# Performance work log

Measured on AMD Instinct MI355X. Metric: run time of the kernel, lower is better.

The kernel has to match this reference:

```python
import jax, jax.numpy as jnp
import numpy as np

N, E, H, ED = 50000, 400000, 512, 64
BN_EPS = 1e-5


def setup_inputs() -> dict:
    key = jax.random.key(0)
    ks = jax.random.split(key, 8)
    s = lambda d: 1.0 / np.sqrt(d)
    return {
        "x": jax.random.normal(ks[0], (N, H), jnp.float32),
        "edge_attr": jax.random.normal(ks[1], (E, ED), jnp.float32),
        "edge_index": jax.random.randint(ks[2], (2, E), 0, N, jnp.int32),
        # GINEConv edge projection (edge_dim -> hidden_dim)
        "W_e": jax.random.normal(ks[3], (ED, H), jnp.float32) * s(ED),
        "b_e": jnp.zeros((H,), jnp.float32),
        # 2-layer MLP: Linear(H, 2H) -> BN -> SiLU -> Linear(2H, H)
        "W1": jax.random.normal(ks[4], (H, 2 * H), jnp.float32) * s(H),
        "b1": jnp.zeros((2 * H,), jnp.float32),
        "g1": jnp.ones((2 * H,), jnp.float32),
        "beta1": jnp.zeros((2 * H,), jnp.float32),
        "W2": jax.random.normal(ks[5], (2 * H, H), jnp.float32) * s(2 * H),
        "b2": jnp.zeros((H,), jnp.float32),
        # outer BatchNorm(hidden_dim)
        "g2": jnp.ones((H,), jnp.float32),
        "beta2": jnp.zeros((H,), jnp.float32),
        # trainable GIN epsilon (init 0)
        "eps": jnp.zeros((), jnp.float32),
    }


def _bn(h, g, b):
    # training-mode batch norm over the node dimension (biased variance)
    mu = jnp.mean(h, axis=0)
    var = jnp.mean(jnp.square(h - mu), axis=0)
    return (h - mu) * jax.lax.rsqrt(var + BN_EPS) * g + b


def reference(x, edge_attr, edge_index, W_e, b_e, W1, b1, g1, beta1, W2, b2, g2, beta2, eps):
    src, dst = edge_index[0], edge_index[1]
    # message: ReLU(x_j + lin(e_ij)), gathered per edge  -> [E, H]
    msg = jax.nn.relu(x[src] + edge_attr @ W_e + b_e)
    # scatter-add aggregate into destination nodes -> [N, H]
    aggr = jax.ops.segment_sum(msg, dst, num_segments=x.shape[0])
    # GIN combine + 2-layer MLP with internal BatchNorm + SiLU (dropout=0)
    h = (1.0 + eps) * x + aggr
    h = jax.nn.silu(_bn(h @ W1 + b1, g1, beta1))
    h = h @ W2 + b2
    # outer BatchNorm + SiLU (dropout=0 -> identity)
    return jax.nn.silu(_bn(h, g2, beta2))
```

## Files before the change

kernel.cpp:

```cpp
#include <hip/hip_runtime.h>
#include <math.h>

#define NN 50000
#define NE 400000
#define HD 512
#define EDIM 64
#define H2 1024
#define LDT 72
#define CAP_SLOT 1200000
#define CAP_TILE 75000
#define CAP_HEAVY 8192
#define NBLK_SCAN 98

typedef short s16x8 __attribute__((ext_vector_type(8)));
typedef float f32x4 __attribute__((ext_vector_type(4)));

__device__ __forceinline__ unsigned short f2bf(float f) {
    union { float f; unsigned u; } v; v.f = f;
    unsigned r = v.u + 0x7fffu + ((v.u >> 16) & 1u);
    return (unsigned short)(r >> 16);
}
__device__ __forceinline__ float bf2f(unsigned short h) {
    union { unsigned u; float f; } v; v.u = ((unsigned)h) << 16;
    return v.f;
}
__device__ __forceinline__ float silu_f(float t) {
    return t / (1.f + __expf(-t));
}

constexpr size_t OFF_AGGRC = 0;
constexpr size_t OFF_XB   = 16777216;
constexpr size_t OFF_H1   = 0;
constexpr size_t OFF_H    = 102400000;
constexpr size_t OFF_WET  = 153600000;
constexpr size_t OFF_W1T  = OFF_WET + 65536;
constexpr size_t OFF_W2T  = OFF_W1T + 1048576;
constexpr size_t OFF_CNT  = OFF_W2T + 1048576;
constexpr size_t OFF_B1S  = OFF_CNT + 200000;
constexpr size_t OFF_B1Q  = OFF_B1S + 4096;
constexpr size_t OFF_B2S  = OFF_B1Q + 4096;
constexpr size_t OFF_B2Q  = OFF_B2S + 2048;
constexpr size_t ZERO_BYTES = 200000 + 4096 + 4096 + 2048 + 2048;
constexpr size_t OFF_TEX  = OFF_B2Q + 2048;
constexpr size_t OFF_BSUM = OFF_TEX + 200000;
constexpr size_t OFF_BOFF = OFF_BSUM + 512;
constexpr size_t OFF_T    = OFF_BOFF + 512;
constexpr size_t OFF_CUR  = OFF_T + 64;
constexpr size_t OFF_NOT  = OFF_CUR + 200000;
constexpr size_t OFF_SRCP = OFF_NOT + 300032;
constexpr size_t OFF_EIXP = OFF_SRCP + 4800000;
constexpr size_t OFF_SC1  = OFF_EIXP + 4800000;
constexpr size_t OFF_SB1  = OFF_SC1 + 4096;
constexpr size_t OFF_SC2  = OFF_SB1 + 4096;
constexpr size_t OFF_SB2  = OFF_SC2 + 2048;

__global__ __launch_bounds__(256) void k_convert(const float* __restrict__ We,
    const float* __restrict__ W1, const float* __restrict__ W2,
    unsigned short* __restrict__ wet, unsigned short* __restrict__ w1t,
    unsigned short* __restrict__ w2t) {
    int i = blockIdx.x * 256 + threadIdx.x;
    if (i < 32768) {
        int n = i >> 6, k = i & 63;
        wet[i] = f2bf(We[k * HD + n]);
    } else if (i < 32768 + 524288) {
        int j = i - 32768;
        int n = j >> 9, k = j & 511;
        w1t[j] = f2bf(W1[k * H2 + n]);
    } else if (i < 32768 + 2 * 524288) {
        int j = i - (32768 + 524288);
        int n = j >> 10, k = j & 1023;
        w2t[j] = f2bf(W2[k * HD + n]);
    }
}

__global__ __launch_bounds__(256) void k_xconv(const float* __restrict__ x,
    unsigned short* __restrict__ xb) {
    int t = blockIdx.x * 256 + threadIdx.x;
    if (t >= NN * 64) return;
    int n = t >> 6, rem = t & 63;
    int cb = rem >> 4, l = rem & 15;
    const float* src = x + (size_t)n * HD + cb * 128 + l;
    unsigned short o[8];
    #pragma unroll
    for (int j = 0; j < 8; ++j) o[j] = f2bf(src[j * 16]);
    *(uint4*)(xb + (size_t)n * HD + cb * 128 + l * 8) = *(const uint4*)o;
}

__global__ __launch_bounds__(256) void k_hist(const int* __restrict__ dst, int* __restrict__ counts) {
    int e = blockIdx.x * 256 + threadIdx.x;
    if (e < NE) atomicAdd(&counts[dst[e]], 1);
}

__global__ __launch_bounds__(512) void k_scan1(const int* __restrict__ counts,
    int* __restrict__ tile_excl, int* __restrict__ bsum) {
    __shared__ int wsums[8];
    int b = blockIdx.x, t = threadIdx.x;
    int i = b * 512 + t;
    int v = (i < NN) ? ((counts[i] + 15) >> 4) : 0;
    int lane = t & 63, wid = t >> 6;
    int x = v;
    #pragma unroll
    for (int o = 1; o < 64; o <<= 1) {
        int y = __shfl_up(x, o, 64);
        if (lane >= o) x += y;
    }
    if (lane == 63) wsums[wid] = x;
    __syncthreads();
    if (t == 0) {
        int run = 0;
        for (int w = 0; w < 8; ++w) { int tmp = wsums[w]; wsums[w] = run; run += tmp; }
    }
    __syncthreads();
    int excl = x - v + wsums[wid];
    if (i < NN) tile_excl[i] = excl;
    if (t == 511) bsum[b] = excl + v;
}

__global__ void k_scan2(const int* __restrict__ bsum, int* __restrict__ boff, int* __restrict__ Tout) {
    if (threadIdx.x == 0) {
        int run = 0;
        for (int b = 0; b < NBLK_SCAN; ++b) { boff[b] = run; run += bsum[b]; }
        Tout[0] = run;
        Tout[1] = 0;
    }
}

__global__ __launch_bounds__(512) void k_scan3(const int* __restrict__ counts,
    int* __restrict__ tile_excl, const int* __restrict__ boff,
    int* __restrict__ cursor, int* __restrict__ node_of_tile, int* __restrict__ Tout) {
    int b = blockIdx.x, t = threadIdx.x;
    int i = b * 512 + t;
    if (i >= NN) return;
    int tc = (counts[i] + 15) >> 4;
    int ts = tile_excl[i] + boff[b];
    cursor[i] = ts * 16;
    int hid = -1;
    if (tc > 1) {
        hid = atomicAdd(&Tout[1], 1);
        if (hid >= CAP_HEAVY) hid = CAP_HEAVY - 1;
    }
    tile_excl[i] = hid;
    unsigned tag = (tc > 1) ? (0x80000000u | (unsigned)hid) : (unsigned)i;
    for (int k = 0; k < tc; ++k) node_of_tile[ts + k] = (int)tag;
}

__global__ __launch_bounds__(256) void k_scatter(const int* __restrict__ src, const int* __restrict__ dst,
    int* __restrict__ cursor, int* __restrict__ srcp, int* __restrict__ eidxp) {
    int e = blockIdx.x * 256 + threadIdx.x;
    if (e < NE) {
        int d = dst[e];
        int p = atomicAdd(&cursor[d], 1);
        srcp[p] = src[e];
        eidxp[p] = e;
    }
}

__global__ __launch_bounds__(256, 4) void k_edge(
    const float* __restrict__ ea, const unsigned short* __restrict__ wet,
    const unsigned short* __restrict__ xb, const float* __restrict__ b_e,
    const float* __restrict__ eps,
    const int* __restrict__ srcp, const int* __restrict__ eidxp,
    const int* __restrict__ node_of_tile, const int* __restrict__ Tptr,
    float* __restrict__ aggrc, unsigned short* __restrict__ h) {
    int tile0 = blockIdx.x * 2;
    int T = Tptr[0];
    if (tile0 >= T) return;
    __shared__ unsigned short As[32 * LDT];
    __shared__ int Ss[32];
    __shared__ float Rs[4][128];
    int t = threadIdx.x;
    int slot0 = tile0 * 16;
    {
        int r = t >> 3, qq = t & 7;
        int s = srcp[slot0 + r];
        if (qq == 0) Ss[r] = s;
        unsigned short* lp = As + r * LDT + qq * 8;
        if (s >= 0) {
            int eix = eidxp[slot0 + r];
            const float* gp = ea + (size_t)eix * EDIM + qq * 8;
            float4 v0 = ((const float4*)gp)[0];
            float4 v1 = ((const float4*)gp)[1];
            lp[0] = f2bf(v0.x); lp[1] = f2bf(v0.y); lp[2] = f2bf(v0.z); lp[3] = f2bf(v0.w);
            lp[4] = f2bf(v1.x); lp[5] = f2bf(v1.y); lp[6] = f2bf(v1.z); lp[7] = f2bf(v1.w);
        } else {
            uint4 z = {0u, 0u, 0u, 0u};
            *(uint4*)lp = z;
        }
    }
    __syncthreads();
    int wave = t >> 6, lane = t & 63, l15 = lane & 15, quad = lane >> 4;
    int cblk = wave * 128;
    f32x4 acc[2][8];
    #pragma unroll
    for (int i = 0; i < 2; ++i)
        #pragma unroll
        for (int j = 0; j < 8; ++j) acc[i][j] = (f32x4){0.f, 0.f, 0.f, 0.f};
    #pragma unroll
    for (int k0 = 0; k0 < 64; k0 += 32) {
        s16x8 af[2], bfr[8];
        #pragma unroll
        for (int i = 0; i < 2; ++i)
            af[i] = *(const s16x8*)(As + (i * 16 + l15) * LDT + k0 + quad * 8);
        #pragma unroll
        for (int j = 0; j < 8; ++j)
            bfr[j] = *(const s16x8*)(wet + (size_t)(cblk + j * 16 + l15) * EDIM + k0 + quad * 8);
        #pragma unroll
        for (int i = 0; i < 2; ++i)
            #pragma unroll
            for (int j = 0; j < 8; ++j)
                acc[i][j] = __builtin_amdgcn_mfma_f32_16x16x32_bf16(af[i], bfr[j], acc[i][j], 0, 0, 0);
    }
    float ep = 1.0f + eps[0];
    float bev[8];
    #pragma unroll
    for (int j = 0; j < 8; ++j) bev[j] = b_e[cblk + j * 16 + l15];
    float* rp = Rs[wave];
    #pragma unroll
    for (int i = 0; i < 2; ++i) {
        int tile = tile0 + i;
        unsigned meta = (unsigned)node_of_tile[tile];
        int v = (int)(meta & 0x7fffffffu);
        int vc = v < NN ? v : 0;
        int srow = i * 16 + quad * 4;
        s16x8 xr[4]; float msk[4];
        #pragma unroll
        for (int r = 0; r < 4; ++r) {
            int s = Ss[srow + r];
            msk[r] = s >= 0 ? 1.f : 0.f;
            xr[r] = *(const s16x8*)(xb + (size_t)(s >= 0 ? s : 0) * HD + cblk + l15 * 8);
        }
        s16x8 xo = *(const s16x8*)(xb + (size_t)vc * HD + cblk + l15 * 8);
        float sum8[8];
        #pragma unroll
        for (int j = 0; j < 8; ++j) sum8[j] = 0.f;
        #pragma unroll
        for (int r = 0; r < 4; ++r) {
            #pragma unroll
            for (int j = 0; j < 8; ++j) {
                float vv = acc[i][j][r] + bf2f((unsigned short)xr[r][j]) + bev[j];
                vv = vv > 0.f ? vv : 0.f;
                sum8[j] = fmaf(msk[r], vv, sum8[j]);
            }
        }
        #pragma unroll
        for (int j = 0; j < 8; ++j) {
            sum8[j] += __shfl_xor(sum8[j], 16, 64);
            sum8[j] += __shfl_xor(sum8[j], 32, 64);
        }
        if (tile < T) {
            if (meta & 0x80000000u) {
                if (quad == 0) {
                    float* ap = aggrc + (size_t)v * HD + cblk;
                    #pragma unroll
                    for (int j = 0; j < 8; ++j) atomicAdd(ap + j * 16 + l15, sum8[j]);
                }
            } else {
                int j0 = quad * 2, j1 = j0 + 1;
                rp[j0 * 16 + l15] = fmaf(ep, bf2f((unsigned short)xo[j0]), sum8[j0]);
                rp[j1 * 16 + l15] = fmaf(ep, bf2f((unsigned short)xo[j1]), sum8[j1]);
                unsigned pk = (unsigned)f2bf(rp[lane * 2]) |
                              ((unsigned)f2bf(rp[lane * 2 + 1]) << 16);
                *(unsigned*)(h + (size_t)v * HD + cblk + lane * 2) = pk;
            }
        }
    }
}

__global__ __launch_bounds__(256) void k_combine_heavy(const float* __restrict__ aggrc,
    const float* __restrict__ x, const int* __restrict__ counts, const int* __restrict__ hidmap,
    const float* __restrict__ eps, unsigned short* __restrict__ h) {
    long i = ((long)blockIdx.x * 256 + threadIdx.x) * 4;
    if (i >= (long)NN * HD) return;
    int v = (int)(i >> 9);
    int c = counts[v];
    if (c >= 1 && c <= 16) return;
    float ep = 1.0f + eps[0];
    float4 a = {0.f, 0.f, 0.f, 0.f};
    if (c > 16) a = *(const float4*)(aggrc + (size_t)hidmap[v] * HD + (i & (HD - 1)));
    float4 xv = *(const float4*)(x + i);
    uint2 p;
    p.x = (unsigned)f2bf(ep * xv.x + a.x) | ((unsigned)f2bf(ep * xv.y + a.y) << 16);
    p.y = (unsigned)f2bf(ep * xv.z + a.z) | ((unsigned)f2bf(ep * xv.w + a.w) << 16);
    *(uint2*)(h + i) = p;
}

template <bool BF16OUT, bool SILU_A>
__global__ __launch_bounds__(256) void k_gemm_bn(
    const unsigned short* __restrict__ A, const unsigned short* __restrict__ Bt,
    const float* __restrict__ bias, void* __restrict__ Cv,
    float* __restrict__ bn_sum, float* __restrict__ bn_sumsq,
    const float* __restrict__ a_sc, const float* __restrict__ a_sb,
    int M, int K, int Nn) {
    __shared__ unsigned short As[128 * LDT];
    __shared__ unsigned short Bs[128 * LDT];
    __shared__ float csum[128], csumsq[128];
    int mblk = blockIdx.x, nblk = blockIdx.y;
    int t = threadIdx.x;
    int row0 = mblk * 128, col0 = nblk * 128;
    int wid = t >> 6, lane = t & 63, l15 = lane & 15, quad = lane >> 4;
    f32x4 acc[2][8];
    #pragma unroll
    for (int i = 0; i < 2; ++i)
        #pragma unroll
        for (int j = 0; j < 8; ++j) acc[i][j] = (f32x4){0.f, 0.f, 0.f, 0.f};

    for (int k0 = 0; k0 < K; k0 += 64) {
        __syncthreads();
        {
            int r = t >> 1, half = t & 1;
            int row = row0 + r;
            int kb = k0 + half * 32;
            unsigned short* lp = As + r * LDT + half * 32;
            if (row < M) {
                const unsigned short* gp = A + (size_t)row * K + kb;
                if (SILU_A) {
                    #pragma unroll
                    for (int jj = 0; jj < 4; ++jj) {
                        uint4 u = *(const uint4*)(gp + jj * 8);
                        float4 sA = *(const float4*)(a_sc + kb + jj * 8);
                        float4 sB = *(const float4*)(a_sc + kb + jj * 8 + 4);
                        float4 bA = *(const float4*)(a_sb + kb + jj * 8);
                        float4 bB = *(const float4*)(a_sb + kb + jj * 8 + 4);
                        unsigned short o[8];
                        o[0] = f2bf(silu_f(bf2f((unsigned short)(u.x & 0xffffu)) * sA.x + bA.x));
                        o[1] = f2bf(silu_f(bf2f((unsigned short)(u.x >> 16)) * sA.y + bA.y));
                        o[2] = f2bf(silu_f(bf2f((unsigned short)(u.y & 0xffffu)) * sA.z + bA.z));
                        o[3] = f2bf(silu_f(bf2f((unsigned short)(u.y >> 16)) * sA.w + bA.w));
                        o[4] = f2bf(silu_f(bf2f((unsigned short)(u.z & 0xffffu)) * sB.x + bB.x));
                        o[5] = f2bf(silu_f(bf2f((unsigned short)(u.z >> 16)) * sB.y + bB.y));
                        o[6] = f2bf(silu_f(bf2f((unsigned short)(u.w & 0xffffu)) * sB.z + bB.z));
                        o[7] = f2bf(silu_f(bf2f((unsigned short)(u.w >> 16)) * sB.w + bB.w));
                        #pragma unroll
                        for (int m = 0; m < 8; ++m) lp[jj * 8 + m] = o[m];
                    }
                } else {
                    #pragma unroll
                    for (int jj = 0; jj < 4; ++jj) *(uint4*)(lp + jj * 8) = *(const uint4*)(gp + jj * 8);
                }
            } else {
                uint4 z = {0u, 0u, 0u, 0u};
                #pragma unroll
                for (int jj = 0; jj < 4; ++jj) *(uint4*)(lp + jj * 8) = z;
            }
            const unsigned short* gb = Bt + (size_t)(col0 + r) * K + kb;
            unsigned short* lb = Bs + r * LDT + half * 32;
            #pragma unroll
            for (int jj = 0; jj < 4; ++jj) *(uint4*)(lb + jj * 8) = *(const uint4*)(gb + jj * 8);
        }
        __syncthreads();
        #pragma unroll
        for (int kk = 0; kk < 64; kk += 32) {
            s16x8 af[2], bfr[8];
            #pragma unroll
            for (int i = 0; i < 2; ++i)
                af[i] = *(const s16x8*)(As + (wid * 32 + i * 16 + l15) * LDT + kk + quad * 8);
            #pragma unroll
            for (int j = 0; j < 8; ++j)
                bfr[j] = *(const s16x8*)(Bs + (j * 16 + l15) * LDT + kk + quad * 8);
            #pragma unroll
            for (int i = 0; i < 2; ++i)
                #pragma unroll
                for (int j = 0; j < 8; ++j)
                    acc[i][j] = __builtin_amdgcn_mfma_f32_16x16x32_bf16(af[i], bfr[j], acc[i][j], 0, 0, 0);
        }
    }
    if (t < 128) { csum[t] = 0.f; csumsq[t] = 0.f; }
    __syncthreads();
    int mrow0 = row0 + wid * 32;
    #pragma unroll
    for (int j = 0; j < 8; ++j) {
        int col = j * 16 + l15;
        float bv = bias[col0 + col];
        float ls = 0.f, lq = 0.f;
        #pragma unroll
        for (int i = 0; i < 2; ++i) {
            #pragma unroll
            for (int r = 0; r < 4; ++r) {
                int row = mrow0 + i * 16 + quad * 4 + r;
                if (row < M) {
                    float v = acc[i][j][r] + bv;
                    if (BF16OUT)
                        ((unsigned short*)Cv)[(size_t)row * Nn + col0 + col] = f2bf(v);
                    else
                        ((float*)Cv)[(size_t)row * Nn + col0 + col] = v;
                    ls += v; lq += v * v;
                }
            }
        }
        atomicAdd(&csum[col], ls);
        atomicAdd(&csumsq[col], lq);
    }
    __syncthreads();
    if (t < 128) {
        atomicAdd(bn_sum + col0 + t, csum[t]);
        atomicAdd(bn_sumsq + col0 + t, csumsq[t]);
    }
}

__global__ __launch_bounds__(256) void k_bn_final(const float* __restrict__ s,
    const float* __restrict__ q, const float* __restrict__ g, const float* __restrict__ beta,
    float* __restrict__ scale, float* __restrict__ sbias, int C, float invN) {
    int c = blockIdx.x * 256 + threadIdx.x;
    if (c < C) {
        float mu = s[c] * invN;
        float var = q[c] * invN - mu * mu;
        var = fmaxf(var, 0.f);
        float sc = g[c] * rsqrtf(var + 1e-5f);
        scale[c] = sc;
        sbias[c] = beta[c] - mu * sc;
    }
}

__global__ __launch_bounds__(256) void k_out(float* __restrict__ out,
    const float* __restrict__ sc, const float* __restrict__ sb, long total) {
    long i = ((long)blockIdx.x * 256 + threadIdx.x) * 4;
    if (i >= total) return;
    int c = (int)(i & (HD - 1));
    float4 v = *(const float4*)(out + i);
    float4 s4 = *(const float4*)(sc + c);
    float4 b4 = *(const float4*)(sb + c);
    float4 o;
    o.x = silu_f(v.x * s4.x + b4.x);
    o.y = silu_f(v.y * s4.y + b4.y);
    o.z = silu_f(v.z * s4.z + b4.z);
    o.w = silu_f(v.w * s4.w + b4.w);
    *(float4*)(out + i) = o;
}

extern "C" void kernel_launch(void* const* d_in, const int* in_sizes, int n_in,
                              void* d_out, int out_size, void* d_ws, size_t ws_size,
                              hipStream_t stream) {
    const float* x      = (const float*)d_in[0];
    const float* ea     = (const float*)d_in[1];
    const int*   ei     = (const int*)d_in[2];
    const float* W_e    = (const float*)d_in[3];
    const float* b_e    = (const float*)d_in[4];
    const float* W1     = (const float*)d_in[5];
    const float* b1     = (const float*)d_in[6];
    const float* g1     = (const float*)d_in[7];
    const float* beta1  = (const float*)d_in[8];
    const float* W2     = (const float*)d_in[9];
    const float* b2     = (const float*)d_in[10];
    const float* g2     = (const float*)d_in[11];
    const float* beta2  = (const float*)d_in[12];
    const float* eps    = (const float*)d_in[13];
    float* out = (float*)d_out;
    char* ws = (char*)d_ws;

    float*          aggrc = (float*)(ws + OFF_AGGRC);
    unsigned short* xb   = (unsigned short*)(ws + OFF_XB);
    unsigned short* h1   = (unsigned short*)(ws + OFF_H1);
    unsigned short* h    = (unsigned short*)(ws + OFF_H);
    unsigned short* wet  = (unsigned short*)(ws + OFF_WET);
    unsigned short* w1t  = (unsigned short*)(ws + OFF_W1T);
    unsigned short* w2t  = (unsigned short*)(ws + OFF_W2T);
    int* counts  = (int*)(ws + OFF_CNT);
    float* b1s   = (float*)(ws + OFF_B1S);
    float* b1q   = (float*)(ws + OFF_B1Q);
    float* b2s   = (float*)(ws + OFF_B2S);
    float* b2q   = (float*)(ws + OFF_B2Q);
    int* tex     = (int*)(ws + OFF_TEX);
    int* bsum    = (int*)(ws + OFF_BSUM);
    int* boff    = (int*)(ws + OFF_BOFF);
    int* Tptr    = (int*)(ws + OFF_T);
    int* cursor  = (int*)(ws + OFF_CUR);
    int* notile  = (int*)(ws + OFF_NOT);
    int* srcp    = (int*)(ws + OFF_SRCP);
    int* eidxp   = (int*)(ws + OFF_EIXP);
    float* sc1   = (float*)(ws + OFF_SC1);
    float* sb1   = (float*)(ws + OFF_SB1);
    float* sc2   = (float*)(ws + OFF_SC2);
    float* sb2   = (float*)(ws + OFF_SB2);

    hipMemsetAsync(aggrc, 0, (size_t)CAP_HEAVY * HD * 4, stream);
    hipMemsetAsync(ws + OFF_CNT, 0, ZERO_BYTES, stream);
    hipMemsetAsync(srcp, 0xFF, (size_t)CAP_SLOT * 4, stream);
    k_convert<<<4224, 256, 0, stream>>>(W_e, W1, W2, wet, w1t, w2t);
    k_xconv<<<(NN * 64 + 255) / 256, 256, 0, stream>>>(x, xb);
    k_hist<<<(NE + 255) / 256, 256, 0, stream>>>(ei + NE, counts);
    k_scan1<<<NBLK_SCAN, 512, 0, stream>>>(counts, tex, bsum);
    k_scan2<<<1, 64, 0, stream>>>(bsum, boff, Tptr);
    k_scan3<<<NBLK_SCAN, 512, 0, stream>>>(counts, tex, boff, cursor, notile, Tptr);
    k_scatter<<<(NE + 255) / 256, 256, 0, stream>>>(ei, ei + NE, cursor, srcp, eidxp);
    k_edge<<<CAP_TILE / 2, 256, 0, stream>>>(ea, wet, xb, b_e, eps, srcp, eidxp, notile, Tptr, aggrc, h);
    k_combine_heavy<<<(int)(((long)NN * HD / 4 + 255) / 256), 256, 0, stream>>>(
        aggrc, x, counts, tex, eps, h);
    k_gemm_bn<true, false><<<dim3((NN + 127) / 128, H2 / 128), 256, 0, stream>>>(
        h, w1t, b1, h1, b1s, b1q, nullptr, nullptr, NN, HD, H2);
    k_bn_final<<<4, 256, 0, stream>>>(b1s, b1q, g1, beta1, sc1, sb1, H2, 1.f / NN);
    k_gemm_bn<false, true><<<dim3((NN + 127) / 128, HD / 128), 256, 0, stream>>>(
        h1, w2t, b2, out, b2s, b2q, sc1, sb1, NN, H2, HD);
    k_bn_final<<<2, 256, 0, stream>>>(b2s, b2q, g2, beta2, sc2, sb2, HD, 1.f / NN);
    k_out<<<(int)(((long)NN * HD / 4 + 255) / 256), 256, 0, stream>>>(out, sc2, sb2, (long)NN * HD);
}
```

Baseline: 996.4 us.

## Make edge kernel persistent with double-buffered LDS prefetch of next tile pair

```diff
diff --git a/kernel.cpp b/kernel.cpp
--- a/kernel.cpp
+++ b/kernel.cpp
@@ -11,6 +11,7 @@
 #define CAP_TILE 75000
 #define CAP_HEAVY 8192
 #define NBLK_SCAN 98
+#define EDGE_BLKS 2048
 
 typedef short s16x8 __attribute__((ext_vector_type(8)));
 typedef float f32x4 __attribute__((ext_vector_type(4)));
@@ -155,31 +156,40 @@
     }
 }
 
-__global__ __launch_bounds__(256, 4) void k_edge(
+__global__ __launch_bounds__(256, 3) void k_edge(
     const float* __restrict__ ea, const unsigned short* __restrict__ wet,
     const unsigned short* __restrict__ xb, const float* __restrict__ b_e,
     const float* __restrict__ eps,
     const int* __restrict__ srcp, const int* __restrict__ eidxp,
     const int* __restrict__ node_of_tile, const int* __restrict__ Tptr,
     float* __restrict__ aggrc, unsigned short* __restrict__ h) {
-    int tile0 = blockIdx.x * 2;
     int T = Tptr[0];
-    if (tile0 >= T) return;
-    __shared__ unsigned short As[32 * LDT];
-    __shared__ int Ss[32];
+    int npair = (T + 1) >> 1;
+    int p = blockIdx.x;
+    if (p >= npair) return;
+    __shared__ unsigned short As[2][32 * LDT];
+    __shared__ int Ss[2][32];
     __shared__ float Rs[4][128];
     int t = threadIdx.x;
-    int slot0 = tile0 * 16;
+    int wave = t >> 6, lane = t & 63, l15 = lane & 15, quad = lane >> 4;
+    int cblk = wave * 128;
+    int r8 = t >> 3, q8 = t & 7;
+    float ep = 1.0f + eps[0];
+    float bev[8];
+    #pragma unroll
+    for (int j = 0; j < 8; ++j) bev[j] = b_e[cblk + j * 16 + l15];
+
     {
-        int r = t >> 3, qq = t & 7;
-        int s = srcp[slot0 + r];
-        if (qq == 0) Ss[r] = s;
-        unsigned short* lp = As + r * LDT + qq * 8;
+        int slot = p * 32 + r8;
+        int s = srcp[slot];
+        int eix = eidxp[slot];
+        if (s < 0) eix = 0;
+        const float* gp = ea + (size_t)eix * EDIM + q8 * 8;
+        float4 v0 = ((const float4*)gp)[0];
+        float4 v1 = ((const float4*)gp)[1];
+        if (q8 == 0) Ss[0][r8] = s;
+        unsigned short* lp = As[0] + r8 * LDT + q8 * 8;
         if (s >= 0) {
-            int eix = eidxp[slot0 + r];
-            const float* gp = ea + (size_t)eix * EDIM + qq * 8;
-            float4 v0 = ((const float4*)gp)[0];
-            float4 v1 = ((const float4*)gp)[1];
             lp[0] = f2bf(v0.x); lp[1] = f2bf(v0.y); lp[2] = f2bf(v0.z); lp[3] = f2bf(v0.w);
             lp[4] = f2bf(v1.x); lp[5] = f2bf(v1.y); lp[6] = f2bf(v1.z); lp[7] = f2bf(v1.w);
         } else {
@@ -188,81 +198,113 @@
         }
     }
     __syncthreads();
-    int wave = t >> 6, lane = t & 63, l15 = lane & 15, quad = lane >> 4;
-    int cblk = wave * 128;
-    f32x4 acc[2][8];
-    #pragma unroll
-    for (int i = 0; i < 2; ++i)
-        #pragma unroll
-        for (int j = 0; j < 8; ++j) acc[i][j] = (f32x4){0.f, 0.f, 0.f, 0.f};
-    #pragma unroll
-    for (int k0 = 0; k0 < 64; k0 += 32) {
-        s16x8 af[2], bfr[8];
+
+    int cur = 0;
+    for (;;) {
+        int pn = p + EDGE_BLKS;
+        bool has_next = pn < npair;
+        int sn = -1, eixn = 0;
+        float4 n0, n1;
+        if (has_next) {
+            int slot = pn * 32 + r8;
+            sn = srcp[slot];
+            eixn = eidxp[slot];
+            if (sn < 0) eixn = 0;
+            const float* gp = ea + (size_t)eixn * EDIM + q8 * 8;
+            n0 = ((const float4*)gp)[0];
+            n1 = ((const float4*)gp)[1];
+        }
+        f32x4 acc[2][8];
         #pragma unroll
         for (int i = 0; i < 2; ++i)
-            af[i] = *(const s16x8*)(As + (i * 16 + l15) * LDT + k0 + quad * 8);
-        #pragma unroll
-        for (int j = 0; j < 8; ++j)
-            bfr[j] = *(const s16x8*)(wet + (size_t)(cblk + j * 16 + l15) * EDIM + k0 + quad * 8);
-        #pragma unroll
-        for (int i = 0; i < 2; ++i)
+            #pragma unroll
+            for (int j = 0; j < 8; ++j) acc[i][j] = (f32x4){0.f, 0.f, 0.f, 0.f};
+        #pragma unroll
+        for (int k0 = 0; k0 < 64; k0 += 32) {
+            s16x8 af[2], bfr[8];
+            #pragma unroll
+            for (int i = 0; i < 2; ++i)
+                af[i] = *(const s16x8*)(As[cur] + (i * 16 + l15) * LDT + k0 + quad * 8);
             #pragma unroll
             for (int j = 0; j < 8; ++j)
-                acc[i][j] = __builtin_amdgcn_mfma_f32_16x16x32_bf16(af[i], bfr[j], acc[i][j], 0, 0, 0);
-    }
-    float ep = 1.0f + eps[0];
-    float bev[8];
-    #pragma unroll
-    for (int j = 0; j < 8; ++j) bev[j] = b_e[cblk + j * 16 + l15];
-    float* rp = Rs[wave];
-    #pragma unroll
-    for (int i = 0; i < 2; ++i) {
-        int tile = tile0 + i;
-        unsigned meta = (unsigned)node_of_tile[tile];
-        int v = (int)(meta & 0x7fffffffu);
-        int vc = v < NN ? v : 0;
-        int srow = i * 16 + quad * 4;
-        s16x8 xr[4]; float msk[4];
-        #pragma unroll
-        for (int r = 0; r < 4; ++r) {
-            int s = Ss[srow + r];
-            msk[r] = s >= 0 ? 1.f : 0.f;
-            xr[r] = *(const s16x8*)(xb + (size_t)(s >= 0 ? s : 0) * HD + cblk + l15 * 8);
-        }
-        s16x8 xo = *(const s16x8*)(xb + (size_t)vc * HD + cblk + l15 * 8);
-        float sum8[8];
-        #pragma unroll
-        for (int j = 0; j < 8; ++j) sum8[j] = 0.f;
-        #pragma unroll
-        for (int r = 0; r < 4; ++r) {
+                bfr[j] = *(const s16x8*)(wet + (size_t)(cblk + j * 16 + l15) * EDIM + k0 + quad * 8);
+            #pragma unroll
+            for (int i = 0; i < 2; ++i)
+                #pragma unroll
+                for (int j = 0; j < 8; ++j)
+                    acc[i][j] = __builtin_amdgcn_mfma_f32_16x16x32_bf16(af[i], bfr[j], acc[i][j], 0, 0, 0);
+        }
+        int tile0 = p * 2;
+        unsigned meta[2]; int vv[2];
+        s16x8 xr[2][4], xo[2];
+        float msk[2][4];
+        #pragma unroll
+        for (int i = 0; i < 2; ++i) {
+            meta[i] = (unsigned)node_of_tile[tile0 + i];
+            int v = (int)(meta[i] & 0x7fffffffu);
+            vv[i] = v;
+            int vc = v < NN ? v : 0;
+            xo[i] = *(const s16x8*)(xb + (size_t)vc * HD + cblk + l15 * 8);
+            int srow = i * 16 + quad * 4;
+            #pragma unroll
+            for (int r = 0; r < 4; ++r) {
+                int s = Ss[cur][srow + r];
+                msk[i][r] = s >= 0 ? 1.f : 0.f;
+                xr[i][r] = *(const s16x8*)(xb + (size_t)(s >= 0 ? s : 0) * HD + cblk + l15 * 8);
+            }
+        }
+        float* rp = Rs[wave];
+        #pragma unroll
+        for (int i = 0; i < 2; ++i) {
+            float sum8[8];
+            #pragma unroll
+            for (int j = 0; j < 8; ++j) sum8[j] = 0.f;
+            #pragma unroll
+            for (int r = 0; r < 4; ++r) {
+                #pragma unroll
+                for (int j = 0; j < 8; ++j) {
+                    float vfv = acc[i][j][r] + bf2f((unsigned short)xr[i][r][j]) + bev[j];
+                    vfv = vfv > 0.f ? vfv : 0.f;
+                    sum8[j] = fmaf(msk[i][r], vfv, sum8[j]);
+                }
+            }
             #pragma unroll
             for (int j = 0; j < 8; ++j) {
-                float vv = acc[i][j][r] + bf2f((unsigned short)xr[r][j]) + bev[j];
-                vv = vv > 0.f ? vv : 0.f;
-                sum8[j] = fmaf(msk[r], vv, sum8[j]);
-            }
-        }
-        #pragma unroll
-        for (int j = 0; j < 8; ++j) {
-            sum8[j] += __shfl_xor(sum8[j], 16, 64);
-            sum8[j] += __shfl_xor(sum8[j], 32, 64);
-        }
-        if (tile < T) {
-            if (meta & 0x80000000u) {
-                if (quad == 0) {
-                    float* ap = aggrc + (size_t)v * HD + cblk;
-                    #pragma unroll
-                    for (int j = 0; j < 8; ++j) atomicAdd(ap + j * 16 + l15, sum8[j]);
+                sum8[j] += __shfl_xor(sum8[j], 16, 64);
+                sum8[j] += __shfl_xor(sum8[j], 32, 64);
+            }
+            if (tile0 + i < T) {
+                if (meta[i] & 0x80000000u) {
+                    if (quad == 0) {
+                        float* ap = aggrc + (size_t)vv[i] * HD + cblk;
+                        #pragma unroll
+                        for (int j = 0; j < 8; ++j) atomicAdd(ap + j * 16 + l15, sum8[j]);
+                    }
+                } else {
+                    int j0 = quad * 2, j1 = j0 + 1;
+                    rp[j0 * 16 + l15] = fmaf(ep, bf2f((unsigned short)xo[i][j0]), sum8[j0]);
+                    rp[j1 * 16 + l15] = fmaf(ep, bf2f((unsigned short)xo[i][j1]), sum8[j1]);
+                    unsigned pk = (unsigned)f2bf(rp[lane * 2]) |
+                                  ((unsigned)f2bf(rp[lane * 2 + 1]) << 16);
+                    *(unsigned*)(h + (size_t)vv[i] * HD + cblk + lane * 2) = pk;
                 }
+            }
+        }
+        if (has_next) {
+            if (q8 == 0) Ss[cur ^ 1][r8] = sn;
+            unsigned short* lp = As[cur ^ 1] + r8 * LDT + q8 * 8;
+            if (sn >= 0) {
+                lp[0] = f2bf(n0.x); lp[1] = f2bf(n0.y); lp[2] = f2bf(n0.z); lp[3] = f2bf(n0.w);
+                lp[4] = f2bf(n1.x); lp[5] = f2bf(n1.y); lp[6] = f2bf(n1.z); lp[7] = f2bf(n1.w);
             } else {
-                int j0 = quad * 2, j1 = j0 + 1;
-                rp[j0 * 16 + l15] = fmaf(ep, bf2f((unsigned short)xo[j0]), sum8[j0]);
-                rp[j1 * 16 + l15] = fmaf(ep, bf2f((unsigned short)xo[j1]), sum8[j1]);
-                unsigned pk = (unsigned)f2bf(rp[lane * 2]) |
-                              ((unsigned)f2bf(rp[lane * 2 + 1]) << 16);
-                *(unsigned*)(h + (size_t)v * HD + cblk + lane * 2) = pk;
-            }
-        }
+                uint4 z = {0u, 0u, 0u, 0u};
+                *(uint4*)lp = z;
+            }
+        }
+        __syncthreads();
+        if (!has_next) break;
+        p = pn;
+        cur ^= 1;
     }
 }
 
@@ -482,7 +524,7 @@
     k_scan2<<<1, 64, 0, stream>>>(bsum, boff, Tptr);
     k_scan3<<<NBLK_SCAN, 512, 0, stream>>>(counts, tex, boff, cursor, notile, Tptr);
     k_scatter<<<(NE + 255) / 256, 256, 0, stream>>>(ei, ei + NE, cursor, srcp, eidxp);
-    k_edge<<<CAP_TILE / 2, 256, 0, stream>>>(ea, wet, xb, b_e, eps, srcp, eidxp, notile, Tptr, aggrc, h);
+    k_edge<<<EDGE_BLKS, 256, 0, stream>>>(ea, wet, xb, b_e, eps, srcp, eidxp, notile, Tptr, aggrc, h);
     k_combine_heavy<<<(int)(((long)NN * HD / 4 + 255) / 256), 256, 0, stream>>>(
         aggrc, x, counts, tex, eps, h);
     k_gemm_bn<true, false><<<dim3((NN + 127) / 128, H2 / 128), 256, 0, stream>>>(
```

After: 1.237 ms. 1.24x slower.
